# Optimization experiments

Measured on AMD Instinct MI355X. Metric: run time of the kernel, lower is better.

## Reference

```python
import jax, jax.numpy as jnp
import numpy as np

N, E = 50000, 800000
IN_DIM, HID, HEADS, OUT_DIM = 128, 64, 4, 64
NEG_SLOPE = 0.2


def add_self_loops(edge_index, n):
    loops = jnp.arange(n, dtype=edge_index.dtype)
    return jnp.concatenate([edge_index, jnp.stack([loops, loops])], axis=1)


def gat_layer(x, edge_index, W, att_src, att_dst, bias, heads, ch, concat):
    n = x.shape[0]
    xp = (x @ W).reshape(n, heads, ch)                       # [N,H,C]
    s_src = jnp.sum(xp * att_src, axis=-1)                   # [N,H]
    s_dst = jnp.sum(xp * att_dst, axis=-1)                   # [N,H]
    src, dst = edge_index[0], edge_index[1]
    e = jax.nn.leaky_relu(s_src[src] + s_dst[dst], NEG_SLOPE)  # [E,H]
    # segment softmax over incoming edges of each destination node
    m = jax.ops.segment_max(e, dst, num_segments=n)
    e = jnp.exp(e - m[dst])
    denom = jax.ops.segment_sum(e, dst, num_segments=n)
    alpha = e / (denom[dst] + 1e-16)                         # [E,H]
    out = jax.ops.segment_sum(xp[src] * alpha[:, :, None], dst, num_segments=n)  # [N,H,C]
    out = out.reshape(n, heads * ch) if concat else out.mean(axis=1)
    return out + bias


def setup_inputs() -> dict:
    key = jax.random.key(0)
    ks = jax.random.split(key, 10)
    glorot = lambda k, shape: jax.random.normal(k, shape, jnp.float32) * np.sqrt(2.0 / (shape[0] + shape[-1]))
    return {
        "x": jax.random.normal(ks[0], (N, IN_DIM), jnp.float32),
        "edge_index": jax.random.randint(ks[1], (2, E), 0, N, jnp.int32),
        "W1": glorot(ks[2], (IN_DIM, HEADS * HID)),
        "att_src1": glorot(ks[3], (HEADS, HID)),
        "att_dst1": glorot(ks[4], (HEADS, HID)),
        "bias1": jnp.zeros((HEADS * HID,), jnp.float32),
        "W2": glorot(ks[5], (HEADS * HID, OUT_DIM)),
        "att_src2": glorot(ks[6], (1, OUT_DIM)),
        "att_dst2": glorot(ks[7], (1, OUT_DIM)),
        "bias2": jnp.zeros((OUT_DIM,), jnp.float32),
    }


def reference(x, edge_index, W1, att_src1, att_dst1, bias1, W2, att_src2, att_dst2, bias2):
    ei = add_self_loops(edge_index, x.shape[0])
    h = gat_layer(x, ei, W1, att_src1, att_dst1, bias1, HEADS, HID, concat=True)
    h = jax.nn.relu(h)
    out = gat_layer(h, ei, W2, att_src2, att_dst2, bias2, 1, OUT_DIM, concat=False)
    return out
```

## Files before the change

### kernel.cpp

```cpp
#include <hip/hip_runtime.h>
#include <hip/hip_bf16.h>
#include <hip/hip_fp16.h>

#define NODES 50000
#define NEDGE 800000
#define NE2   850000
#define INDIM 128
#define F1    256
#define HEADS 4
#define HID   64
#define OUTD  64
#define MTILES 3125

#define NB   196
#define PB   196
#define EPB  4096
#define CAP  6144
#define G1B  782

typedef _Float16 f16;
typedef _Float16 f16x8 __attribute__((ext_vector_type(8)));
typedef float    f32x4 __attribute__((ext_vector_type(4)));

__device__ __forceinline__ float lrelu_exp(float e) {
    e = e > 0.f ? e : 0.2f * e;
    return __expf(e);
}

__global__ void k_hist(const int* __restrict__ ei, int* __restrict__ blkhist,
                       const float* __restrict__ W1, const float* __restrict__ W2,
                       f16* __restrict__ W1p, f16* __restrict__ W2p)
{
    const int b = blockIdx.x, t = threadIdx.x;
    if (b < PB) {
        __shared__ int h[NB];
        for (int i = t; i < NB; i += 256) h[i] = 0;
        __syncthreads();
        const int e0 = b * EPB;
        const int eend = min(e0 + EPB, NEDGE);
        for (int i = e0 + t; i < eend; i += 256) {
            int d = ei[NEDGE + i];
            atomicAdd(&h[d >> 8], 1);
        }
        __syncthreads();
        for (int i = t; i < NB; i += 256) blkhist[i * PB + b] = h[i];
    } else {
        int idx = (b - PB) * 256 + t;
        if (idx < 32768) {
            int j = idx & 7, l = (idx >> 3) & 63, fi = idx >> 9;
            int kb = fi & 3, ct = fi >> 2;
            int k = kb * 32 + (l >> 4) * 8 + j;
            int col = ct * 16 + (l & 15);
            W1p[idx] = (f16)W1[k * F1 + col];
        } else {
            int i2 = idx - 32768;
            int j = i2 & 7, l = (i2 >> 3) & 63, fi = i2 >> 9;
            int kb = fi & 7, ct = fi >> 3;
            int k = kb * 32 + (l >> 4) * 8 + j;
            int col = ct * 16 + (l & 15);
            W2p[i2] = (f16)W2[k * OUTD + col];
        }
    }
}

__global__ void k_part(const int* __restrict__ ei, const int* __restrict__ blkhist,
                       int* __restrict__ rowtot, unsigned* __restrict__ staged)
{
    const int b = blockIdx.x, t = threadIdx.x;
    __shared__ int sS[256];
    __shared__ int cur[NB];
    int rowsum = 0, colpref = 0;
    if (t < NB) {
        const int* hrow = blkhist + t * PB;
        for (int p = 0; p < PB; ++p) {
            int h = hrow[p];
            colpref += (p < b) ? h : 0;
            rowsum += h;
        }
        if (b == 0) rowtot[t] = rowsum;
    }
    sS[t] = (t < NB) ? rowsum : 0;
    __syncthreads();
    for (int off = 1; off < 256; off <<= 1) {
        int tv = (t >= off) ? sS[t - off] : 0;
        __syncthreads();
        sS[t] += tv;
        __syncthreads();
    }
    if (t < NB) cur[t] = (sS[t] - rowsum) + colpref;
    __syncthreads();
    const int e0 = b * EPB;
    const int eend = min(e0 + EPB, NEDGE);
    for (int i = e0 + t; i < eend; i += 256) {
        int sN = ei[i];
        int d  = ei[NEDGE + i];
        int pos = atomicAdd(&cur[d >> 8], 1);
        staged[pos] = (unsigned)sN | ((unsigned)(d & 255) << 16);
    }
}

__global__ __launch_bounds__(256) void k_bg(
    const unsigned* __restrict__ staged, const int* __restrict__ rowtot,
    int* __restrict__ row_ptr, int* __restrict__ csr_src,
    const float* __restrict__ x, const f16* __restrict__ W1p,
    const float* __restrict__ as1, const float* __restrict__ ad1,
    f16* __restrict__ xp1h, float* __restrict__ ssrc, float* __restrict__ sdst)
{
    if (blockIdx.x < NB) {
        __shared__ unsigned sorted2[CAP];
        __shared__ int bin[256];
        __shared__ int cnt[256];
        __shared__ int sh[256];
        __shared__ int ssum[4];
        const int q = blockIdx.x, t = threadIdx.x;
        const int wv = t >> 6, lane = t & 63;
        int pv = (t < q) ? rowtot[t] : 0;
#pragma unroll
        for (int off = 32; off; off >>= 1) pv += __shfl_xor(pv, off);
        if (lane == 0) ssum[wv] = pv;
        cnt[t] = 0; bin[t] = 0;
        __syncthreads();
        const int estart = ssum[0] + ssum[1] + ssum[2] + ssum[3];
        const int m = rowtot[q];
        const int nodebase = q * 256;
        const int nn = min(256, NODES - nodebase);
        const int csrbase = estart + nodebase;

        const bool dosort = (m <= CAP);
        if (dosort) {
            for (int i = t; i < m; i += 256)
                atomicAdd(&bin[(staged[estart + i] & 0xFFFFu) >> 8], 1);
            __syncthreads();
            int bv = bin[t];
            sh[t] = bv;
            __syncthreads();
            for (int off = 1; off < 256; off <<= 1) {
                int tv = (t >= off) ? sh[t - off] : 0;
                __syncthreads();
                sh[t] += tv;
                __syncthreads();
            }
            bin[t] = sh[t] - bv;
            __syncthreads();
            for (int i = t; i < m; i += 256) {
                unsigned u = staged[estart + i];
                int p = atomicAdd(&bin[(u & 0xFFFFu) >> 8], 1);
                sorted2[p] = u;
            }
            __syncthreads();
        }

        if (dosort) {
            for (int i = t; i < m; i += 256)
                atomicAdd(&cnt[sorted2[i] >> 16], 1);
        } else {
            for (int i = t; i < m; i += 256)
                atomicAdd(&cnt[staged[estart + i] >> 16], 1);
        }
        __syncthreads();
        int v = cnt[t];
        sh[t] = v;
        __syncthreads();
        for (int off = 1; off < 256; off <<= 1) {
            int tv = (t >= off) ? sh[t - off] : 0;
            __syncthreads();
            sh[t] += tv;
            __syncthreads();
        }
        int excl = sh[t] - v;
        __syncthreads();
        if (t < nn) {
            int r = csrbase + excl + t;
            row_ptr[nodebase + t] = r;
            csr_src[r] = nodebase + t;
            cnt[t] = excl + t + 1;
        }
        __syncthreads();
        if (dosort) {
            for (int i = t; i < m; i += 256) {
                unsigned u = sorted2[i];
                int pos = atomicAdd(&cnt[u >> 16], 1);
                csr_src[csrbase + pos] = (int)(u & 0xFFFFu);
            }
        } else {
            for (int i = t; i < m; i += 256) {
                unsigned u = staged[estart + i];
                int pos = atomicAdd(&cnt[u >> 16], 1);
                csr_src[csrbase + pos] = (int)(u & 0xFFFFu);
            }
        }
        if (q == NB - 1 && t == 0) row_ptr[NODES] = NE2;
        return;
    }

    const int wv = threadIdx.x >> 6, lane = threadIdx.x & 63;
    const int l15 = lane & 15, quad = lane >> 4;
    const int rowtile = (blockIdx.x - NB) * 4 + wv;
    if (rowtile >= MTILES) return;
    const int rowbase = rowtile * 16;

    f16x8 afrag[4];
    const float* xrow = x + (rowbase + l15) * INDIM + quad * 8;
#pragma unroll
    for (int kb = 0; kb < 4; ++kb) {
        float4 u0 = *(const float4*)(xrow + kb * 32);
        float4 u1 = *(const float4*)(xrow + kb * 32 + 4);
        f16x8 a;
        a[0] = (f16)u0.x; a[1] = (f16)u0.y; a[2] = (f16)u0.z; a[3] = (f16)u0.w;
        a[4] = (f16)u1.x; a[5] = (f16)u1.y; a[6] = (f16)u1.z; a[7] = (f16)u1.w;
        afrag[kb] = a;
    }

    const f16x8* Wf = (const f16x8*)W1p;
    f32x4 acc[16];
#pragma unroll
    for (int ct = 0; ct < 16; ++ct) acc[ct] = (f32x4){0.f, 0.f, 0.f, 0.f};
#pragma unroll
    for (int ct = 0; ct < 16; ++ct) {
#pragma unroll
        for (int kb = 0; kb < 4; ++kb) {
            f16x8 b = Wf[(ct * 4 + kb) * 64 + lane];
            acc[ct] = __builtin_amdgcn_mfma_f32_16x16x32_f16(afrag[kb], b, acc[ct], 0, 0, 0);
        }
    }
    const int orow = rowbase + quad * 4;
#pragma unroll
    for (int ct = 0; ct < 16; ++ct) {
#pragma unroll
        for (int r = 0; r < 4; ++r)
            xp1h[(orow + r) * F1 + ct * 16 + l15] = (f16)acc[ct][r];
    }
    float ps[4][4], pd[4][4];
#pragma unroll
    for (int h = 0; h < 4; ++h)
#pragma unroll
        for (int r = 0; r < 4; ++r) { ps[h][r] = 0.f; pd[h][r] = 0.f; }
#pragma unroll
    for (int ct = 0; ct < 16; ++ct) {
        float av = as1[ct * 16 + l15];
        float dv = ad1[ct * 16 + l15];
        int h = ct >> 2;
#pragma unroll
        for (int r = 0; r < 4; ++r) {
            ps[h][r] = fmaf(acc[ct][r], av, ps[h][r]);
            pd[h][r] = fmaf(acc[ct][r], dv, pd[h][r]);
        }
    }
#pragma unroll
    for (int off = 8; off; off >>= 1) {
#pragma unroll
        for (int h = 0; h < 4; ++h)
#pragma unroll
            for (int r = 0; r < 4; ++r) {
                ps[h][r] += __shfl_xor(ps[h][r], off);
                pd[h][r] += __shfl_xor(pd[h][r], off);
            }
    }
    if (l15 == 0) {
#pragma unroll
        for (int r = 0; r < 4; ++r) {
            int row = orow + r;
            float4 vs = {ps[0][r], ps[1][r], ps[2][r], ps[3][r]};
            float4 vd = {pd[0][r], pd[1][r], pd[2][r], pd[3][r]};
            ((float4*)ssrc)[row] = vs;
            ((float4*)sdst)[row] = vd;
        }
    }
}

__global__ __launch_bounds__(256) void k_agg1(
    const int* __restrict__ row_ptr, const int* __restrict__ csr_src,
    const float* __restrict__ ssrc, const float* __restrict__ sdst,
    const f16* __restrict__ xp1h, const float* __restrict__ bias,
    f16* __restrict__ hbuf)
{
    const int wv = threadIdx.x >> 6, l = threadIdx.x & 63;
    const int n = blockIdx.x * 4 + wv;
    const int g = l >> 4, sub = l & 15;
    const int hlo = sub >> 3;
    const float sdl = sdst[n * HEADS + hlo];
    const float sdh = sdst[n * HEADS + 2 + hlo];
    const int jbeg = row_ptr[n], jend = row_ptr[n + 1];
    const f16x8* xv = (const f16x8*)xp1h;

    float denl = 0.f, denh = 0.f;
    float alo[8] = {0.f,0.f,0.f,0.f,0.f,0.f,0.f,0.f};
    float ahi[8] = {0.f,0.f,0.f,0.f,0.f,0.f,0.f,0.f};

    for (int e = jbeg + g; e < jend; e += 8) {
        const int e2 = e + 4;
        const bool vb = (e2 < jend);
        int sa = csr_src[e];
        int sb = vb ? csr_src[e2] : 0;
        float scal = ssrc[sa * HEADS + hlo];
        float scah = ssrc[sa * HEADS + 2 + hlo];
        f16x8 va0 = xv[sa * 32 + sub];
        f16x8 va1 = xv[sa * 32 + sub + 16];
        float scbl = ssrc[sb * HEADS + hlo];
        float scbh = ssrc[sb * HEADS + 2 + hlo];
        f16x8 vb0 = xv[sb * 32 + sub];
        f16x8 vb1 = xv[sb * 32 + sub + 16];
        float eal = lrelu_exp(scal + sdl);
        float eah = lrelu_exp(scah + sdh);
        float ebl = vb ? lrelu_exp(scbl + sdl) : 0.f;
        float ebh = vb ? lrelu_exp(scbh + sdh) : 0.f;
        denl += eal + ebl;
        denh += eah + ebh;
#pragma unroll
        for (int j = 0; j < 8; ++j) {
            alo[j] = fmaf(eal, (float)va0[j], alo[j]);
            ahi[j] = fmaf(eah, (float)va1[j], ahi[j]);
        }
#pragma unroll
        for (int j = 0; j < 8; ++j) {
            alo[j] = fmaf(ebl, (float)vb0[j], alo[j]);
            ahi[j] = fmaf(ebh, (float)vb1[j], ahi[j]);
        }
    }
    denl += __shfl_xor(denl, 16); denl += __shfl_xor(denl, 32);
    denh += __shfl_xor(denh, 16); denh += __shfl_xor(denh, 32);
    const float rdl = 1.f / (denl + 1e-16f);
    const float rdh = 1.f / (denh + 1e-16f);
#pragma unroll
    for (int j = 0; j < 8; ++j) {
        alo[j] += __shfl_xor(alo[j], 16); alo[j] += __shfl_xor(alo[j], 32);
        ahi[j] += __shfl_xor(ahi[j], 16); ahi[j] += __shfl_xor(ahi[j], 32);
    }
    if (g == 0) {
        const float4* b4 = (const float4*)bias;
        float4 bl0 = b4[sub * 2],        bl1 = b4[sub * 2 + 1];
        float4 bh0 = b4[(sub + 16) * 2], bh1 = b4[(sub + 16) * 2 + 1];
        f16x8 olo, ohi;
        float v;
        v = fmaf(alo[0], rdl, bl0.x); olo[0] = (f16)(v > 0.f ? v : 0.f);
        v = fmaf(alo[1], rdl, bl0.y); olo[1] = (f16)(v > 0.f ? v : 0.f);
        v = fmaf(alo[2], rdl, bl0.z); olo[2] = (f16)(v > 0.f ? v : 0.f);
        v = fmaf(alo[3], rdl, bl0.w); olo[3] = (f16)(v > 0.f ? v : 0.f);
        v = fmaf(alo[4], rdl, bl1.x); olo[4] = (f16)(v > 0.f ? v : 0.f);
        v = fmaf(alo[5], rdl, bl1.y); olo[5] = (f16)(v > 0.f ? v : 0.f);
        v = fmaf(alo[6], rdl, bl1.z); olo[6] = (f16)(v > 0.f ? v : 0.f);
        v = fmaf(alo[7], rdl, bl1.w); olo[7] = (f16)(v > 0.f ? v : 0.f);
        v = fmaf(ahi[0], rdh, bh0.x); ohi[0] = (f16)(v > 0.f ? v : 0.f);
        v = fmaf(ahi[1], rdh, bh0.y); ohi[1] = (f16)(v > 0.f ? v : 0.f);
        v = fmaf(ahi[2], rdh, bh0.z); ohi[2] = (f16)(v > 0.f ? v : 0.f);
        v = fmaf(ahi[3], rdh, bh0.w); ohi[3] = (f16)(v > 0.f ? v : 0.f);
        v = fmaf(ahi[4], rdh, bh1.x); ohi[4] = (f16)(v > 0.f ? v : 0.f);
        v = fmaf(ahi[5], rdh, bh1.y); ohi[5] = (f16)(v > 0.f ? v : 0.f);
        v = fmaf(ahi[6], rdh, bh1.z); ohi[6] = (f16)(v > 0.f ? v : 0.f);
        v = fmaf(ahi[7], rdh, bh1.w); ohi[7] = (f16)(v > 0.f ? v : 0.f);
        ((f16x8*)hbuf)[n * 32 + sub] = olo;
        ((f16x8*)hbuf)[n * 32 + sub + 16] = ohi;
    }
}

__global__ __launch_bounds__(256) void k_gemm2m(
    const f16* __restrict__ hbuf, const f16* __restrict__ W2p,
    const float* __restrict__ as2, const float* __restrict__ ad2,
    f16* __restrict__ xp2h, float* __restrict__ ssrc, float* __restrict__ sdst)
{
    const int wv = threadIdx.x >> 6, lane = threadIdx.x & 63;
    const int l15 = lane & 15, quad = lane >> 4;
    const int rowtile = blockIdx.x * 4 + wv;
    if (rowtile >= MTILES) return;
    const int rowbase = rowtile * 16;

    const f16x8* Wf = (const f16x8*)W2p;
    f32x4 acc[4];
#pragma unroll
    for (int ct = 0; ct < 4; ++ct) acc[ct] = (f32x4){0.f, 0.f, 0.f, 0.f};
    const f16* hrow = hbuf + (rowbase + l15) * F1 + quad * 8;
#pragma unroll
    for (int kb = 0; kb < 8; ++kb) {
        f16x8 a = *(const f16x8*)(hrow + kb * 32);
#pragma unroll
        for (int ct = 0; ct < 4; ++ct) {
            f16x8 b = Wf[(ct * 8 + kb) * 64 + lane];
            acc[ct] = __builtin_amdgcn_mfma_f32_16x16x32_f16(a, b, acc[ct], 0, 0, 0);
        }
    }
    const int orow = rowbase + quad * 4;
#pragma unroll
    for (int ct = 0; ct < 4; ++ct) {
#pragma unroll
        for (int r = 0; r < 4; ++r)
            xp2h[(orow + r) * OUTD + ct * 16 + l15] = (f16)acc[ct][r];
    }
    float ps[4] = {0.f,0.f,0.f,0.f}, pd[4] = {0.f,0.f,0.f,0.f};
#pragma unroll
    for (int ct = 0; ct < 4; ++ct) {
        float av = as2[ct * 16 + l15];
        float dv = ad2[ct * 16 + l15];
#pragma unroll
        for (int r = 0; r < 4; ++r) {
            ps[r] = fmaf(acc[ct][r], av, ps[r]);
            pd[r] = fmaf(acc[ct][r], dv, pd[r]);
        }
    }
#pragma unroll
    for (int off = 8; off; off >>= 1) {
#pragma unroll
        for (int r = 0; r < 4; ++r) {
            ps[r] += __shfl_xor(ps[r], off);
            pd[r] += __shfl_xor(pd[r], off);
        }
    }
    if (l15 == 0) {
#pragma unroll
        for (int r = 0; r < 4; ++r) {
            ssrc[orow + r] = ps[r];
            sdst[orow + r] = pd[r];
        }
    }
}

__global__ __launch_bounds__(256) void k_agg2(
    const int* __restrict__ row_ptr, const int* __restrict__ csr_src,
    const float* __restrict__ ssrc, const float* __restrict__ sdst,
    const f16* __restrict__ xp2h, const float* __restrict__ bias,
    float* __restrict__ out)
{
    const int wv = threadIdx.x >> 6, l = threadIdx.x & 63;
    const int n = blockIdx.x * 4 + wv;
    const int grp = l >> 3, sub = l & 7;
    const float sd = sdst[n];
    const int jbeg = row_ptr[n], jend = row_ptr[n + 1];
    const f16x8* xv = (const f16x8*)xp2h;

    float den = 0.f;
    float acc[8] = {0.f,0.f,0.f,0.f,0.f,0.f,0.f,0.f};
    for (int e = jbeg + grp; e < jend; e += 16) {
        const int e2 = e + 8;
        const bool vb = (e2 < jend);
        int sa = csr_src[e];
        int sb = vb ? csr_src[e2] : 0;
        float sca = ssrc[sa];
        float scb = ssrc[sb];
        f16x8 va = xv[sa * 8 + sub];
        f16x8 vbx = xv[sb * 8 + sub];
        float ea = lrelu_exp(sca + sd);
        float eb = vb ? lrelu_exp(scb + sd) : 0.f;
        den += ea + eb;
#pragma unroll
        for (int j = 0; j < 8; ++j) acc[j] = fmaf(ea, (float)va[j], acc[j]);
#pragma unroll
        for (int j = 0; j < 8; ++j) acc[j] = fmaf(eb, (float)vbx[j], acc[j]);
    }
    den += __shfl_xor(den, 8);
    den += __shfl_xor(den, 16);
    den += __shfl_xor(den, 32);
    const float rd = 1.f / (den + 1e-16f);
#pragma unroll
    for (int j = 0; j < 8; ++j) {
        acc[j] += __shfl_xor(acc[j], 8);
        acc[j] += __shfl_xor(acc[j], 16);
        acc[j] += __shfl_xor(acc[j], 32);
    }
    if (grp == 0) {
        const float4* b4 = (const float4*)bias;
        float4 ba = b4[sub * 2], bb = b4[sub * 2 + 1];
        float4 o0, o1;
        o0.x = fmaf(acc[0], rd, ba.x); o0.y = fmaf(acc[1], rd, ba.y);
        o0.z = fmaf(acc[2], rd, ba.z); o0.w = fmaf(acc[3], rd, ba.w);
        o1.x = fmaf(acc[4], rd, bb.x); o1.y = fmaf(acc[5], rd, bb.y);
        o1.z = fmaf(acc[6], rd, bb.z); o1.w = fmaf(acc[7], rd, bb.w);
        float4* ov = (float4*)out + n * 16 + sub * 2;
        ov[0] = o0; ov[1] = o1;
    }
}

extern "C" void kernel_launch(void* const* d_in, const int* in_sizes, int n_in,
                              void* d_out, int out_size, void* d_ws, size_t ws_size,
                              hipStream_t stream)
{
    (void)in_sizes; (void)n_in; (void)out_size; (void)ws_size;
    const float* x   = (const float*)d_in[0];
    const int*   ei  = (const int*)d_in[1];
    const float* W1  = (const float*)d_in[2];
    const float* as1 = (const float*)d_in[3];
    const float* ad1 = (const float*)d_in[4];
    const float* b1  = (const float*)d_in[5];
    const float* W2  = (const float*)d_in[6];
    const float* as2 = (const float*)d_in[7];
    const float* ad2 = (const float*)d_in[8];
    const float* b2  = (const float*)d_in[9];
    float* out = (float*)d_out;

    f16* xp1h    = (f16*)d_ws;
    f16* hbuf    = xp1h + (size_t)NODES * F1;
    f16* W1p     = hbuf + (size_t)NODES * F1;
    f16* W2p     = W1p + 32768;
    float* ssrc1 = (float*)(W2p + 16384);
    float* sdst1 = ssrc1 + (size_t)NODES * HEADS;
    float* ssrc2 = sdst1 + (size_t)NODES * HEADS;
    float* sdst2 = ssrc2 + (size_t)NODES;
    int* row_ptr = (int*)(sdst2 + (size_t)NODES);
    int* blkhist = row_ptr + NODES + 1;
    int* rowtot  = blkhist + NB * PB;
    int* csr_src = rowtot + NB;
    unsigned* staged = (unsigned*)(csr_src + NE2);
    f16* xp2h    = xp1h;

    k_hist<<<PB + 192, 256, 0, stream>>>(ei, blkhist, W1, W2, W1p, W2p);
    k_part<<<PB, 256, 0, stream>>>(ei, blkhist, rowtot, staged);

    k_bg<<<NB + G1B, 256, 0, stream>>>(staged, rowtot, row_ptr, csr_src,
                                       x, W1p, as1, ad1, xp1h, ssrc1, sdst1);

    k_agg1<<<NODES / 4, 256, 0, stream>>>(row_ptr, csr_src, ssrc1, sdst1,
                                          xp1h, b1, hbuf);

    k_gemm2m<<<(MTILES + 3) / 4, 256, 0, stream>>>(hbuf, W2p, as2, ad2,
                                                   xp2h, ssrc2, sdst2);
    k_agg2<<<NODES / 4, 256, 0, stream>>>(row_ptr, csr_src, ssrc2, sdst2,
                                          xp2h, b2, out);
}
```

Measured before the change: 229.1 us.

## Split feature tables into column planes and slice aggregation per plane

The projected features for both layers are stored as column-sliced planes (32 halfs per node per plane for layer 1, 16 for layer 2), and the attention scores as head-major arrays. Each aggregation block now handles one plane for four nodes, so each gather reads a small contiguous chunk from a plane that fits better in cache, and there are 8x or 4x more blocks. The cost is that the edge indices and exp scores are recomputed once per slice, and the gathers become narrower, less vectorized loads. The edge index loads are marked nontemporal.

```diff
diff --git a/kernel.cpp b/kernel.cpp
--- a/kernel.cpp
+++ b/kernel.cpp
@@ -20,6 +20,8 @@
 
 typedef _Float16 f16;
 typedef _Float16 f16x8 __attribute__((ext_vector_type(8)));
+typedef _Float16 f16x4 __attribute__((ext_vector_type(4)));
+typedef _Float16 f16x2 __attribute__((ext_vector_type(2)));
 typedef float    f32x4 __attribute__((ext_vector_type(4)));
 
 __device__ __forceinline__ float lrelu_exp(float e) {
@@ -226,9 +228,11 @@
     const int orow = rowbase + quad * 4;
 #pragma unroll
     for (int ct = 0; ct < 16; ++ct) {
+        f16* plane = xp1h + (size_t)(ct >> 1) * NODES * 32;
+        const int cw = (ct & 1) * 16 + l15;
 #pragma unroll
         for (int r = 0; r < 4; ++r)
-            xp1h[(orow + r) * F1 + ct * 16 + l15] = (f16)acc[ct][r];
+            plane[(orow + r) * 32 + cw] = (f16)acc[ct][r];
     }
     float ps[4][4], pd[4][4];
 #pragma unroll
@@ -260,96 +264,66 @@
 #pragma unroll
         for (int r = 0; r < 4; ++r) {
             int row = orow + r;
-            float4 vs = {ps[0][r], ps[1][r], ps[2][r], ps[3][r]};
-            float4 vd = {pd[0][r], pd[1][r], pd[2][r], pd[3][r]};
-            ((float4*)ssrc)[row] = vs;
-            ((float4*)sdst)[row] = vd;
-        }
-    }
-}
-
-__global__ __launch_bounds__(256) void k_agg1(
+#pragma unroll
+            for (int h = 0; h < 4; ++h) {
+                ssrc[h * NODES + row] = ps[h][r];
+                sdst[h * NODES + row] = pd[h][r];
+            }
+        }
+    }
+}
+
+__global__ __launch_bounds__(256) void k_agg1s(
     const int* __restrict__ row_ptr, const int* __restrict__ csr_src,
     const float* __restrict__ ssrc, const float* __restrict__ sdst,
     const f16* __restrict__ xp1h, const float* __restrict__ bias,
     f16* __restrict__ hbuf)
 {
     const int wv = threadIdx.x >> 6, l = threadIdx.x & 63;
-    const int n = blockIdx.x * 4 + wv;
-    const int g = l >> 4, sub = l & 15;
-    const int hlo = sub >> 3;
-    const float sdl = sdst[n * HEADS + hlo];
-    const float sdh = sdst[n * HEADS + 2 + hlo];
+    const int slice = blockIdx.x & 7;
+    const int n = (blockIdx.x >> 3) * 4 + wv;
+    const int grp = l >> 3, sub = l & 7;
+    const int h = slice >> 1;
+    const float sd = sdst[h * NODES + n];
     const int jbeg = row_ptr[n], jend = row_ptr[n + 1];
-    const f16x8* xv = (const f16x8*)xp1h;
-
-    float denl = 0.f, denh = 0.f;
-    float alo[8] = {0.f,0.f,0.f,0.f,0.f,0.f,0.f,0.f};
-    float ahi[8] = {0.f,0.f,0.f,0.f,0.f,0.f,0.f,0.f};
-
-    for (int e = jbeg + g; e < jend; e += 8) {
-        const int e2 = e + 4;
+    const f16x4* xv = (const f16x4*)(xp1h + (size_t)slice * NODES * 32);
+    const float* sc = ssrc + (size_t)h * NODES;
+
+    float den = 0.f;
+    float a0 = 0.f, a1 = 0.f, a2 = 0.f, a3 = 0.f;
+    for (int e = jbeg + grp; e < jend; e += 16) {
+        const int e2 = e + 8;
         const bool vb = (e2 < jend);
-        int sa = csr_src[e];
-        int sb = vb ? csr_src[e2] : 0;
-        float scal = ssrc[sa * HEADS + hlo];
-        float scah = ssrc[sa * HEADS + 2 + hlo];
-        f16x8 va0 = xv[sa * 32 + sub];
-        f16x8 va1 = xv[sa * 32 + sub + 16];
-        float scbl = ssrc[sb * HEADS + hlo];
-        float scbh = ssrc[sb * HEADS + 2 + hlo];
-        f16x8 vb0 = xv[sb * 32 + sub];
-        f16x8 vb1 = xv[sb * 32 + sub + 16];
-        float eal = lrelu_exp(scal + sdl);
-        float eah = lrelu_exp(scah + sdh);
-        float ebl = vb ? lrelu_exp(scbl + sdl) : 0.f;
-        float ebh = vb ? lrelu_exp(scbh + sdh) : 0.f;
-        denl += eal + ebl;
-        denh += eah + ebh;
-#pragma unroll
-        for (int j = 0; j < 8; ++j) {
-            alo[j] = fmaf(eal, (float)va0[j], alo[j]);
-            ahi[j] = fmaf(eah, (float)va1[j], ahi[j]);
-        }
-#pragma unroll
-        for (int j = 0; j < 8; ++j) {
-            alo[j] = fmaf(ebl, (float)vb0[j], alo[j]);
-            ahi[j] = fmaf(ebh, (float)vb1[j], ahi[j]);
-        }
-    }
-    denl += __shfl_xor(denl, 16); denl += __shfl_xor(denl, 32);
-    denh += __shfl_xor(denh, 16); denh += __shfl_xor(denh, 32);
-    const float rdl = 1.f / (denl + 1e-16f);
-    const float rdh = 1.f / (denh + 1e-16f);
-#pragma unroll
-    for (int j = 0; j < 8; ++j) {
-        alo[j] += __shfl_xor(alo[j], 16); alo[j] += __shfl_xor(alo[j], 32);
-        ahi[j] += __shfl_xor(ahi[j], 16); ahi[j] += __shfl_xor(ahi[j], 32);
-    }
-    if (g == 0) {
-        const float4* b4 = (const float4*)bias;
-        float4 bl0 = b4[sub * 2],        bl1 = b4[sub * 2 + 1];
-        float4 bh0 = b4[(sub + 16) * 2], bh1 = b4[(sub + 16) * 2 + 1];
-        f16x8 olo, ohi;
+        int sa = __builtin_nontemporal_load(csr_src + e);
+        int sb = vb ? __builtin_nontemporal_load(csr_src + e2) : 0;
+        float sca = sc[sa];
+        float scb = sc[sb];
+        f16x4 va  = xv[sa * 8 + sub];
+        f16x4 vbx = xv[sb * 8 + sub];
+        float ea = lrelu_exp(sca + sd);
+        float eb = vb ? lrelu_exp(scb + sd) : 0.f;
+        den += ea + eb;
+        a0 = fmaf(ea, (float)va[0], a0); a1 = fmaf(ea, (float)va[1], a1);
+        a2 = fmaf(ea, (float)va[2], a2); a3 = fmaf(ea, (float)va[3], a3);
+        a0 = fmaf(eb, (float)vbx[0], a0); a1 = fmaf(eb, (float)vbx[1], a1);
+        a2 = fmaf(eb, (float)vbx[2], a2); a3 = fmaf(eb, (float)vbx[3], a3);
+    }
+    den += __shfl_xor(den, 8); den += __shfl_xor(den, 16); den += __shfl_xor(den, 32);
+    const float rd = 1.f / (den + 1e-16f);
+    a0 += __shfl_xor(a0, 8); a0 += __shfl_xor(a0, 16); a0 += __shfl_xor(a0, 32);
+    a1 += __shfl_xor(a1, 8); a1 += __shfl_xor(a1, 16); a1 += __shfl_xor(a1, 32);
+    a2 += __shfl_xor(a2, 8); a2 += __shfl_xor(a2, 16); a2 += __shfl_xor(a2, 32);
+    a3 += __shfl_xor(a3, 8); a3 += __shfl_xor(a3, 16); a3 += __shfl_xor(a3, 32);
+    if (grp == 0) {
+        const int cb = slice * 32 + sub * 4;
+        float4 bb = *(const float4*)(bias + cb);
+        f16x4 o;
         float v;
-        v = fmaf(alo[0], rdl, bl0.x); olo[0] = (f16)(v > 0.f ? v : 0.f);
-        v = fmaf(alo[1], rdl, bl0.y); olo[1] = (f16)(v > 0.f ? v : 0.f);
-        v = fmaf(alo[2], rdl, bl0.z); olo[2] = (f16)(v > 0.f ? v : 0.f);
-        v = fmaf(alo[3], rdl, bl0.w); olo[3] = (f16)(v > 0.f ? v : 0.f);
-        v = fmaf(alo[4], rdl, bl1.x); olo[4] = (f16)(v > 0.f ? v : 0.f);
-        v = fmaf(alo[5], rdl, bl1.y); olo[5] = (f16)(v > 0.f ? v : 0.f);
-        v = fmaf(alo[6], rdl, bl1.z); olo[6] = (f16)(v > 0.f ? v : 0.f);
-        v = fmaf(alo[7], rdl, bl1.w); olo[7] = (f16)(v > 0.f ? v : 0.f);
-        v = fmaf(ahi[0], rdh, bh0.x); ohi[0] = (f16)(v > 0.f ? v : 0.f);
-        v = fmaf(ahi[1], rdh, bh0.y); ohi[1] = (f16)(v > 0.f ? v : 0.f);
-        v = fmaf(ahi[2], rdh, bh0.z); ohi[2] = (f16)(v > 0.f ? v : 0.f);
-        v = fmaf(ahi[3], rdh, bh0.w); ohi[3] = (f16)(v > 0.f ? v : 0.f);
-        v = fmaf(ahi[4], rdh, bh1.x); ohi[4] = (f16)(v > 0.f ? v : 0.f);
-        v = fmaf(ahi[5], rdh, bh1.y); ohi[5] = (f16)(v > 0.f ? v : 0.f);
-        v = fmaf(ahi[6], rdh, bh1.z); ohi[6] = (f16)(v > 0.f ? v : 0.f);
-        v = fmaf(ahi[7], rdh, bh1.w); ohi[7] = (f16)(v > 0.f ? v : 0.f);
-        ((f16x8*)hbuf)[n * 32 + sub] = olo;
-        ((f16x8*)hbuf)[n * 32 + sub + 16] = ohi;
+        v = fmaf(a0, rd, bb.x); o[0] = (f16)(v > 0.f ? v : 0.f);
+        v = fmaf(a1, rd, bb.y); o[1] = (f16)(v > 0.f ? v : 0.f);
+        v = fmaf(a2, rd, bb.z); o[2] = (f16)(v > 0.f ? v : 0.f);
+        v = fmaf(a3, rd, bb.w); o[3] = (f16)(v > 0.f ? v : 0.f);
+        *(f16x4*)(hbuf + (size_t)n * F1 + cb) = o;
     }
 }
 
@@ -381,9 +355,10 @@
     const int orow = rowbase + quad * 4;
 #pragma unroll
     for (int ct = 0; ct < 4; ++ct) {
+        f16* plane = xp2h + (size_t)ct * NODES * 16;
 #pragma unroll
         for (int r = 0; r < 4; ++r)
-            xp2h[(orow + r) * OUTD + ct * 16 + l15] = (f16)acc[ct][r];
+            plane[(orow + r) * 16 + l15] = (f16)acc[ct][r];
     }
     float ps[4] = {0.f,0.f,0.f,0.f}, pd[4] = {0.f,0.f,0.f,0.f};
 #pragma unroll
@@ -413,58 +388,47 @@
     }
 }
 
-__global__ __launch_bounds__(256) void k_agg2(
+__global__ __launch_bounds__(256) void k_agg2s(
     const int* __restrict__ row_ptr, const int* __restrict__ csr_src,
     const float* __restrict__ ssrc, const float* __restrict__ sdst,
     const f16* __restrict__ xp2h, const float* __restrict__ bias,
     float* __restrict__ out)
 {
     const int wv = threadIdx.x >> 6, l = threadIdx.x & 63;
-    const int n = blockIdx.x * 4 + wv;
+    const int slice = blockIdx.x & 3;
+    const int n = (blockIdx.x >> 2) * 4 + wv;
     const int grp = l >> 3, sub = l & 7;
     const float sd = sdst[n];
     const int jbeg = row_ptr[n], jend = row_ptr[n + 1];
-    const f16x8* xv = (const f16x8*)xp2h;
+    const f16x2* xv = (const f16x2*)(xp2h + (size_t)slice * NODES * 16);
 
     float den = 0.f;
-    float acc[8] = {0.f,0.f,0.f,0.f,0.f,0.f,0.f,0.f};
+    float a0 = 0.f, a1 = 0.f;
     for (int e = jbeg + grp; e < jend; e += 16) {
         const int e2 = e + 8;
         const bool vb = (e2 < jend);
-        int sa = csr_src[e];
-        int sb = vb ? csr_src[e2] : 0;
+        int sa = __builtin_nontemporal_load(csr_src + e);
+        int sb = vb ? __builtin_nontemporal_load(csr_src + e2) : 0;
         float sca = ssrc[sa];
         float scb = ssrc[sb];
-        f16x8 va = xv[sa * 8 + sub];
-        f16x8 vbx = xv[sb * 8 + sub];
+        f16x2 va  = xv[sa * 8 + sub];
+        f16x2 vbx = xv[sb * 8 + sub];
         float ea = lrelu_exp(sca + sd);
         float eb = vb ? lrelu_exp(scb + sd) : 0.f;
         den += ea + eb;
-#pragma unroll
-        for (int j = 0; j < 8; ++j) acc[j] = fmaf(ea, (float)va[j], acc[j]);
-#pragma unroll
-        for (int j = 0; j < 8; ++j) acc[j] = fmaf(eb, (float)vbx[j], acc[j]);
-    }
-    den += __shfl_xor(den, 8);
-    den += __shfl_xor(den, 16);
-    den += __shfl_xor(den, 32);
+        a0 = fmaf(ea, (float)va[0], a0); a1 = fmaf(ea, (float)va[1], a1);
+        a0 = fmaf(eb, (float)vbx[0], a0); a1 = fmaf(eb, (float)vbx[1], a1);
+    }
+    den += __shfl_xor(den, 8); den += __shfl_xor(den, 16); den += __shfl_xor(den, 32);
     const float rd = 1.f / (den + 1e-16f);
-#pragma unroll
-    for (int j = 0; j < 8; ++j) {
-        acc[j] += __shfl_xor(acc[j], 8);
-        acc[j] += __shfl_xor(acc[j], 16);
-        acc[j] += __shfl_xor(acc[j], 32);
-    }
+    a0 += __shfl_xor(a0, 8); a0 += __shfl_xor(a0, 16); a0 += __shfl_xor(a0, 32);
+    a1 += __shfl_xor(a1, 8); a1 += __shfl_xor(a1, 16); a1 += __shfl_xor(a1, 32);
     if (grp == 0) {
-        const float4* b4 = (const float4*)bias;
-        float4 ba = b4[sub * 2], bb = b4[sub * 2 + 1];
-        float4 o0, o1;
-        o0.x = fmaf(acc[0], rd, ba.x); o0.y = fmaf(acc[1], rd, ba.y);
-        o0.z = fmaf(acc[2], rd, ba.z); o0.w = fmaf(acc[3], rd, ba.w);
-        o1.x = fmaf(acc[4], rd, bb.x); o1.y = fmaf(acc[5], rd, bb.y);
-        o1.z = fmaf(acc[6], rd, bb.z); o1.w = fmaf(acc[7], rd, bb.w);
-        float4* ov = (float4*)out + n * 16 + sub * 2;
-        ov[0] = o0; ov[1] = o1;
+        const int cb = slice * 16 + sub * 2;
+        float2 o;
+        o.x = fmaf(a0, rd, bias[cb]);
+        o.y = fmaf(a1, rd, bias[cb + 1]);
+        *(float2*)(out + (size_t)n * OUTD + cb) = o;
     }
 }
 
@@ -506,11 +470,11 @@
     k_bg<<<NB + G1B, 256, 0, stream>>>(staged, rowtot, row_ptr, csr_src,
                                        x, W1p, as1, ad1, xp1h, ssrc1, sdst1);
 
-    k_agg1<<<NODES / 4, 256, 0, stream>>>(row_ptr, csr_src, ssrc1, sdst1,
-                                          xp1h, b1, hbuf);
+    k_agg1s<<<(NODES / 4) * 8, 256, 0, stream>>>(row_ptr, csr_src, ssrc1, sdst1,
+                                                 xp1h, b1, hbuf);
 
     k_gemm2m<<<(MTILES + 3) / 4, 256, 0, stream>>>(hbuf, W2p, as2, ad2,
                                                    xp2h, ssrc2, sdst2);
-    k_agg2<<<NODES / 4, 256, 0, stream>>>(row_ptr, csr_src, ssrc2, sdst2,
-                                          xp2h, b2, out);
-}
+    k_agg2s<<<(NODES / 4) * 4, 256, 0, stream>>>(row_ptr, csr_src, ssrc2, sdst2,
+                                                 xp2h, b2, out);
+}
```

Result: slower. 371.7 us (+62.2%).

## Precompute partition offsets in a scan kernel and drop per-bin source sort

Applied to the files above, without the earlier changes.

Adds a small k_scanR kernel that turns each bin's per-block histogram row into exclusive prefix offsets and row totals. k_part then loads its offsets directly instead of having every block re-read the whole 196x196 histogram. k_bg also drops the shared-memory secondary sort by source index, which shrinks its shared memory and removes a scan and a scatter pass. In exchange there is one extra kernel launch, and CSR neighbour lists are no longer ordered by source, which may hurt locality of the gathers in the aggregation kernels.

```diff
diff --git a/kernel.cpp b/kernel.cpp
--- a/kernel.cpp
+++ b/kernel.cpp
@@ -15,7 +15,6 @@
 #define NB   196
 #define PB   196
 #define EPB  4096
-#define CAP  6144
 #define G1B  782
 
 typedef _Float16 f16;
@@ -63,31 +62,37 @@
     }
 }
 
+__global__ void k_scanR(int* __restrict__ blkhist, int* __restrict__ rowtot)
+{
+    __shared__ int sh[256];
+    const int q = blockIdx.x, t = threadIdx.x;
+    int v = (t < PB) ? blkhist[q * PB + t] : 0;
+    sh[t] = v; __syncthreads();
+    for (int off = 1; off < 256; off <<= 1) {
+        int tv = (t >= off) ? sh[t - off] : 0;
+        __syncthreads();
+        sh[t] += tv;
+        __syncthreads();
+    }
+    if (t < PB) blkhist[q * PB + t] = sh[t] - v;
+    if (t == 255) rowtot[q] = sh[255];
+}
+
 __global__ void k_part(const int* __restrict__ ei, const int* __restrict__ blkhist,
-                       int* __restrict__ rowtot, unsigned* __restrict__ staged)
+                       const int* __restrict__ rowtot, unsigned* __restrict__ staged)
 {
     const int b = blockIdx.x, t = threadIdx.x;
     __shared__ int sS[256];
     __shared__ int cur[NB];
-    int rowsum = 0, colpref = 0;
-    if (t < NB) {
-        const int* hrow = blkhist + t * PB;
-        for (int p = 0; p < PB; ++p) {
-            int h = hrow[p];
-            colpref += (p < b) ? h : 0;
-            rowsum += h;
-        }
-        if (b == 0) rowtot[t] = rowsum;
-    }
-    sS[t] = (t < NB) ? rowsum : 0;
-    __syncthreads();
+    int v = (t < NB) ? rowtot[t] : 0;
+    sS[t] = v; __syncthreads();
     for (int off = 1; off < 256; off <<= 1) {
         int tv = (t >= off) ? sS[t - off] : 0;
         __syncthreads();
         sS[t] += tv;
         __syncthreads();
     }
-    if (t < NB) cur[t] = (sS[t] - rowsum) + colpref;
+    if (t < NB) cur[t] = (sS[t] - v) + blkhist[t * PB + b];
     __syncthreads();
     const int e0 = b * EPB;
     const int eend = min(e0 + EPB, NEDGE);
@@ -107,8 +112,6 @@
     f16* __restrict__ xp1h, float* __restrict__ ssrc, float* __restrict__ sdst)
 {
     if (blockIdx.x < NB) {
-        __shared__ unsigned sorted2[CAP];
-        __shared__ int bin[256];
         __shared__ int cnt[256];
         __shared__ int sh[256];
         __shared__ int ssum[4];
@@ -118,45 +121,16 @@
 #pragma unroll
         for (int off = 32; off; off >>= 1) pv += __shfl_xor(pv, off);
         if (lane == 0) ssum[wv] = pv;
-        cnt[t] = 0; bin[t] = 0;
+        cnt[t] = 0;
         __syncthreads();
         const int estart = ssum[0] + ssum[1] + ssum[2] + ssum[3];
-        const int m = rowtot[q];
+        const int eend   = estart + rowtot[q];
         const int nodebase = q * 256;
         const int nn = min(256, NODES - nodebase);
         const int csrbase = estart + nodebase;
 
-        const bool dosort = (m <= CAP);
-        if (dosort) {
-            for (int i = t; i < m; i += 256)
-                atomicAdd(&bin[(staged[estart + i] & 0xFFFFu) >> 8], 1);
-            __syncthreads();
-            int bv = bin[t];
-            sh[t] = bv;
-            __syncthreads();
-            for (int off = 1; off < 256; off <<= 1) {
-                int tv = (t >= off) ? sh[t - off] : 0;
-                __syncthreads();
-                sh[t] += tv;
-                __syncthreads();
-            }
-            bin[t] = sh[t] - bv;
-            __syncthreads();
-            for (int i = t; i < m; i += 256) {
-                unsigned u = staged[estart + i];
-                int p = atomicAdd(&bin[(u & 0xFFFFu) >> 8], 1);
-                sorted2[p] = u;
-            }
-            __syncthreads();
-        }
-
-        if (dosort) {
-            for (int i = t; i < m; i += 256)
-                atomicAdd(&cnt[sorted2[i] >> 16], 1);
-        } else {
-            for (int i = t; i < m; i += 256)
-                atomicAdd(&cnt[staged[estart + i] >> 16], 1);
-        }
+        for (int i = estart + t; i < eend; i += 256)
+            atomicAdd(&cnt[staged[i] >> 16], 1);
         __syncthreads();
         int v = cnt[t];
         sh[t] = v;
@@ -176,18 +150,10 @@
             cnt[t] = excl + t + 1;
         }
         __syncthreads();
-        if (dosort) {
-            for (int i = t; i < m; i += 256) {
-                unsigned u = sorted2[i];
-                int pos = atomicAdd(&cnt[u >> 16], 1);
-                csr_src[csrbase + pos] = (int)(u & 0xFFFFu);
-            }
-        } else {
-            for (int i = t; i < m; i += 256) {
-                unsigned u = staged[estart + i];
-                int pos = atomicAdd(&cnt[u >> 16], 1);
-                csr_src[csrbase + pos] = (int)(u & 0xFFFFu);
-            }
+        for (int i = estart + t; i < eend; i += 256) {
+            unsigned u = staged[i];
+            int pos = atomicAdd(&cnt[u >> 16], 1);
+            csr_src[csrbase + pos] = (int)(u & 0xFFFFu);
         }
         if (q == NB - 1 && t == 0) row_ptr[NODES] = NE2;
         return;
@@ -501,6 +467,7 @@
     f16* xp2h    = xp1h;
 
     k_hist<<<PB + 192, 256, 0, stream>>>(ei, blkhist, W1, W2, W1p, W2p);
+    k_scanR<<<NB, 256, 0, stream>>>(blkhist, rowtot);
     k_part<<<PB, 256, 0, stream>>>(ei, blkhist, rowtot, staged);
 
     k_bg<<<NB + G1B, 256, 0, stream>>>(staged, rowtot, row_ptr, csr_src,
```

Measured after the change: 224.7 us. No clear change (-1.9%).
